# Optimization experiments

Measured on AMD Instinct MI355X. Metric: run time of the kernel, lower is better.

The kernel has to match this reference:

```python
import jax, jax.numpy as jnp
import numpy as np

D = 120000   # sample_size
H1 = 600     # sample_size/200
H2 = 300     # sample_size/400
H3 = 200     # sample_size/600
DENSITY = 0.1  # sparselinear default connectivity
B = 512
EPS = 1e-5

_LAYER_SPECS = [(H1, D), (H1, H1), (H2, H1), (H3, H2), (H3, H3)]


def _make_idx(key, out_d, in_d, nnz):
    k1, k2 = jax.random.split(key)
    rows = jax.random.randint(k1, (nnz,), 0, out_d)
    cols = jax.random.randint(k2, (nnz,), 0, in_d)
    return jnp.stack([rows, cols]).astype(jnp.int32)


def setup_inputs() -> dict:
    key = jax.random.key(0)
    ks = jax.random.split(key, 32)
    inp = {"x": jax.random.normal(ks[0], (B, D), jnp.float32)}
    for i, (o, ii) in enumerate(_LAYER_SPECS, 1):
        nnz = int(DENSITY * o * ii)
        scale = 1.0 / np.sqrt(DENSITY * ii)  # kaiming-like fan-in scaling on nonzeros
        inp[f"idx{i}"] = _make_idx(ks[3 * i], o, ii, nnz)
        inp[f"val{i}"] = jax.random.normal(ks[3 * i + 1], (nnz,), jnp.float32) * scale
        inp[f"b{i}"] = jnp.zeros((o,), jnp.float32)
    for j, d in enumerate([H1, H2, H3], 1):
        inp[f"g{j}"] = jnp.ones((d,), jnp.float32)
        inp[f"be{j}"] = jnp.zeros((d,), jnp.float32)
    return inp


def _sp_linear(x, idx, vals, bias, out_d):
    # COO sparse linear: y = x @ W^T + b, W scattered from (row, col, val)
    in_d = x.shape[1]
    W = jnp.zeros((out_d, in_d), x.dtype).at[idx[0], idx[1]].add(vals)
    return x @ W.T + bias


def _bn(x, g, b):
    # BatchNorm1d, training mode: biased batch variance
    m = x.mean(axis=0)
    v = x.var(axis=0)
    return (x - m) * jax.lax.rsqrt(v + EPS) * g + b


def reference(x, idx1, val1, b1, idx2, val2, b2, idx3, val3, b3,
              idx4, val4, b4, idx5, val5, b5,
              g1, be1, g2, be2, g3, be3):
    h = jax.nn.silu(_bn(_sp_linear(x, idx1, val1, b1, H1), g1, be1))
    h = jax.nn.silu(_sp_linear(h, idx2, val2, b2, H1))
    h = jax.nn.silu(_bn(_sp_linear(h, idx3, val3, b3, H2), g2, be2))
    h = jax.nn.silu(_bn(_sp_linear(h, idx4, val4, b4, H3), g3, be3))
    return _sp_linear(h, idx5, val5, b5, H3)
```

## Files before the change

kernel.cpp:

```cpp
#include <hip/hip_runtime.h>

typedef unsigned short ushort_t;
typedef unsigned int uint_t;

typedef __bf16 bf16x8 __attribute__((ext_vector_type(8)));
typedef float  floatx4 __attribute__((ext_vector_type(4)));

#define AS3 __attribute__((address_space(3)))
#define AS1 __attribute__((address_space(1)))

#define BATCH 512
#define D_IN  120000
#define N1P   640
#define N2P   640
#define N3P   320
#define N4P   256
#define N5P   256

#define KSPLIT 30
#define KCHUNK 4000

#define HALF    60000
#define CHW     15000
#define NREG    1200
#define NB      256
#define RSTRIDE 6912

static constexpr long O_W1 = 0;
static constexpr long SZ_W1 = 640L * 120000 * 2;
static constexpr long O_W2 = O_W1 + SZ_W1;
static constexpr long SZ_W2 = 640L * 640 * 4;
static constexpr long O_W3 = O_W2 + SZ_W2;
static constexpr long SZ_W3 = 320L * 640 * 4;
static constexpr long O_W4 = O_W3 + SZ_W3;
static constexpr long SZ_W4 = 256L * 320 * 4;
static constexpr long O_W5 = O_W4 + SZ_W4;
static constexpr long SZ_W5 = 256L * 256 * 4;
static constexpr long O_Y1 = O_W5 + SZ_W5;
static constexpr long SZ_Y1 = 512L * 640 * 4;
static constexpr long ZERO_OFF = O_W2;
static constexpr long ZERO_BYTES = (O_Y1 + SZ_Y1) - O_W2;
static constexpr long O_XB = O_Y1 + SZ_Y1;
static constexpr long SZ_XB = 512L * 120000 * 2;
static constexpr long O_CNT = O_XB;
static constexpr long O_OFF = O_CNT + (long)NREG * NB * 4;
static constexpr long O_TOT = O_OFF + (long)NB * NREG * 4;
static constexpr long O_REC = O_TOT + 4800;
static constexpr long O_H1 = O_XB;
static constexpr long O_H2 = O_H1 + 512L * 640 * 4;
static constexpr long O_Y3 = O_H2 + 512L * 640 * 4;
static constexpr long O_H3 = O_Y3 + 512L * 320 * 4;
static constexpr long O_Y4 = O_H3 + 512L * 320 * 4;
static constexpr long O_H4 = O_Y4 + 512L * 256 * 4;

__device__ __forceinline__ ushort_t f2bf(float f) {
    union { float f; uint_t u; } x;
    x.f = f;
    uint_t u = x.u;
    return (ushort_t)((u + 0x7FFFu + ((u >> 16) & 1u)) >> 16);
}
__device__ __forceinline__ float silu_f(float z) {
    return z / (1.f + expf(-z));
}
__device__ __forceinline__ void load16_lds(const void* g, void* l) {
    __builtin_amdgcn_global_load_lds((const AS1 char*)g, (AS3 char*)l, 16, 0, 0);
}

__global__ void zero_f4(float4* __restrict__ p, long n4) {
    long stride = (long)gridDim.x * blockDim.x;
    for (long i = (long)blockIdx.x * blockDim.x + threadIdx.x; i < n4; i += stride)
        p[i] = make_float4(0.f, 0.f, 0.f, 0.f);
}

__global__ void cast_f32_bf16(const float* __restrict__ X, ushort_t* __restrict__ Xb, long n8) {
    long t = (long)blockIdx.x * blockDim.x + threadIdx.x;
    if (t >= n8) return;
    const float4* p = (const float4*)X + 2 * t;
    float4 a = p[0], b = p[1];
    union { ushort_t us[8]; uint4 v; } u;
    u.us[0] = f2bf(a.x); u.us[1] = f2bf(a.y); u.us[2] = f2bf(a.z); u.us[3] = f2bf(a.w);
    u.us[4] = f2bf(b.x); u.us[5] = f2bf(b.y); u.us[6] = f2bf(b.z); u.us[7] = f2bf(b.w);
    ((uint4*)Xb)[t] = u.v;
}

__global__ __launch_bounds__(512) void hist1(const int* __restrict__ idx, int nnz, int chunk,
                                             int* __restrict__ counts ) {
    __shared__ uint_t h[NREG];
    const int b = blockIdx.x, t = threadIdx.x;
    for (int i = t; i < NREG; i += 512) h[i] = 0;
    __syncthreads();
    const int s = b * chunk;
    const int e = min(s + chunk, nnz);
    for (int i = s + t; i < e; i += 512) {
        int r = idx[i];
        int c = idx[nnz + i];
        atomicAdd(&h[r * 2 + (c >= HALF ? 1 : 0)], 1u);
    }
    __syncthreads();
    for (int i = t; i < NREG; i += 512) counts[(long)i * NB + b] = (int)h[i];
}

__global__ __launch_bounds__(NB) void scan1(const int* __restrict__ counts ,
                                            int* __restrict__ offs ,
                                            int* __restrict__ totals) {
    __shared__ int s[NB];
    const int reg = blockIdx.x, t = threadIdx.x;
    const int v = counts[(long)reg * NB + t];
    s[t] = v;
    __syncthreads();
    for (int o = 1; o < NB; o <<= 1) {
        int x = (t >= o) ? s[t - o] : 0;
        __syncthreads();
        s[t] += x;
        __syncthreads();
    }
    offs[(long)t * NREG + reg] = s[t] - v;
    if (t == NB - 1) totals[reg] = s[t];
}

__global__ __launch_bounds__(512) void scatter1(const int* __restrict__ idx,
                                                const float* __restrict__ vals,
                                                int nnz, int chunk,
                                                const int* __restrict__ offs ,
                                                int2* __restrict__ rec) {
    __shared__ int cur[NREG];
    const int b = blockIdx.x, t = threadIdx.x;
    const int* ob = offs + (long)b * NREG;
    for (int i = t; i < NREG; i += 512) cur[i] = i * RSTRIDE + ob[i];
    __syncthreads();
    const int s = b * chunk;
    const int e = min(s + chunk, nnz);
    for (int i = s + t; i < e; i += 512) {
        int r = idx[i];
        int c = idx[nnz + i];
        float v = vals[i];
        int h = (c >= HALF) ? 1 : 0;
        int reg = r * 2 + h;
        int slot = atomicAdd(&cur[reg], 1);
        if (slot < (reg + 1) * RSTRIDE)
            rec[slot] = make_int2(c - h * HALF, __float_as_int(v));
    }
}

__global__ __launch_bounds__(512) void build_w1(const int2* __restrict__ rec,
                                                const int* __restrict__ totals,
                                                ushort_t* __restrict__ W) {
    const int bid = blockIdx.x;
    const int r = bid >> 1, h = bid & 1;
    const int t = threadIdx.x;
    ushort_t* dstbase = W + (size_t)r * D_IN + h * HALF;

    if (r >= 600) {
        uint4 z = make_uint4(0, 0, 0, 0);
        for (int j = t * 8; j < HALF; j += 512 * 8) *(uint4*)(dstbase + j) = z;
        return;
    }

    __shared__ int2 lrec[RSTRIDE];
    __shared__ float acc[CHW];

    const int reg = r * 2 + h;
    const int n = min(totals[reg], RSTRIDE);
    const int2* src = rec + (long)reg * RSTRIDE;
    for (int i = t; i < n; i += 512) lrec[i] = src[i];
    __syncthreads();

#pragma unroll
    for (int ch = 0; ch < 4; ch++) {
        for (int j = t * 4; j < CHW; j += 512 * 4)
            *(float4*)&acc[j] = make_float4(0.f, 0.f, 0.f, 0.f);
        __syncthreads();
        const int base = ch * CHW;
        for (int i = t; i < n; i += 512) {
            int2 e = lrec[i];
            unsigned off = (unsigned)(e.x - base);
            if (off < (unsigned)CHW)
                atomicAdd(&acc[off], __int_as_float(e.y));
        }
        __syncthreads();
        ushort_t* dst = dstbase + base;
        for (int j = t * 8; j < CHW; j += 512 * 8) {
            union { ushort_t us[8]; uint4 v; } u;
#pragma unroll
            for (int k = 0; k < 8; k++) u.us[k] = f2bf(acc[j + k]);
            *(uint4*)(dst + j) = u.v;
        }
        __syncthreads();
    }
}

__global__ void scatter_all(const int* __restrict__ i2, const float* __restrict__ v2, int n2,
                            const int* __restrict__ i3, const float* __restrict__ v3, int n3,
                            const int* __restrict__ i4, const float* __restrict__ v4, int n4,
                            const int* __restrict__ i5, const float* __restrict__ v5, int n5,
                            float* __restrict__ W2, float* __restrict__ W3,
                            float* __restrict__ W4, float* __restrict__ W5) {
    int i = blockIdx.x * blockDim.x + threadIdx.x;
    if (i < n2) { atomicAdd(&W2[(size_t)i2[i] * 640 + i2[n2 + i]], v2[i]); return; }
    i -= n2;
    if (i < n3) { atomicAdd(&W3[(size_t)i3[i] * 640 + i3[n3 + i]], v3[i]); return; }
    i -= n3;
    if (i < n4) { atomicAdd(&W4[(size_t)i4[i] * 320 + i4[n4 + i]], v4[i]); return; }
    i -= n4;
    if (i < n5) { atomicAdd(&W5[(size_t)i5[i] * 256 + i5[n5 + i]], v5[i]); }
}

__global__ __launch_bounds__(256) void gemm1(const ushort_t* __restrict__ X,
                                             const ushort_t* __restrict__ W,
                                             float* __restrict__ Y) {
    __shared__ ushort_t sA[3][4096];
    __shared__ ushort_t sB[3][4096];

    const int b = blockIdx.x;
    const int wrk = (b & 7) * 75 + (b >> 3);
    const int ksIdx = wrk / 20;
    const int tile = wrk % 20;
    const int bm = tile / 5, bn = tile % 5;
    const int ks = ksIdx * KCHUNK;
    const int iters = KCHUNK / 32;

    const int t = threadIdx.x;
    const int lane = t & 63;
    const int w = t >> 6;
    const int wm = w >> 1, wn = w & 1;
    const int i16 = lane & 15;
    const int qk = lane >> 4;

    const int row0 = t >> 2;
    const int kq = (t & 3) ^ ((t >> 3) & 3);

    const ushort_t* pa0 = X + (size_t)(bm * 128 + row0) * D_IN + ks + kq * 8;
    const ushort_t* pa1 = pa0 + (size_t)64 * D_IN;
    const ushort_t* pb0 = W + (size_t)(bn * 128 + row0) * D_IN + ks + kq * 8;
    const ushort_t* pb1 = pb0 + (size_t)64 * D_IN;

    int aoff[4], boff[4];
#pragma unroll
    for (int mi = 0; mi < 4; mi++) {
        int row = wm * 64 + mi * 16 + i16;
        aoff[mi] = row * 64 + ((qk ^ ((row >> 1) & 3)) * 16);
    }
#pragma unroll
    for (int ni = 0; ni < 4; ni++) {
        int row = wn * 64 + ni * 16 + i16;
        boff[ni] = row * 64 + ((qk ^ ((row >> 1) & 3)) * 16);
    }
    const char* sAb = (const char*)sA;
    const char* sBb = (const char*)sB;

#define STAGE1(s) do {                                   \
        load16_lds(pa0, &sA[s][(w * 64) * 8]);           \
        load16_lds(pa1, &sA[s][(256 + w * 64) * 8]);     \
        load16_lds(pb0, &sB[s][(w * 64) * 8]);           \
        load16_lds(pb1, &sB[s][(256 + w * 64) * 8]);     \
        pa0 += 32; pa1 += 32; pb0 += 32; pb1 += 32; } while (0)

    floatx4 acc[4][4] = {};

    STAGE1(0);
    STAGE1(1);

    for (int it = 0; it < iters; ++it) {
        if (it < iters - 1) {
            asm volatile("s_waitcnt vmcnt(4)" ::: "memory");
        } else {
            asm volatile("s_waitcnt vmcnt(0)" ::: "memory");
        }
        __builtin_amdgcn_s_barrier();
        __builtin_amdgcn_sched_barrier(0);

        if (it + 2 < iters) {
            const int ns = (it + 2) % 3;
            STAGE1(ns);
        }

        const int cb = it % 3;
        bf16x8 af[4], bfr[4];
#pragma unroll
        for (int mi = 0; mi < 4; mi++)
            af[mi] = *(const bf16x8*)(sAb + cb * 8192 + aoff[mi]);
#pragma unroll
        for (int ni = 0; ni < 4; ni++)
            bfr[ni] = *(const bf16x8*)(sBb + cb * 8192 + boff[ni]);
#pragma unroll
        for (int mi = 0; mi < 4; mi++)
#pragma unroll
            for (int ni = 0; ni < 4; ni++)
                acc[mi][ni] = __builtin_amdgcn_mfma_f32_16x16x32_bf16(af[mi], bfr[ni], acc[mi][ni], 0, 0, 0);
    }
#undef STAGE1

#pragma unroll
    for (int mi = 0; mi < 4; mi++) {
#pragma unroll
        for (int ni = 0; ni < 4; ni++) {
#pragma unroll
            for (int r = 0; r < 4; r++) {
                int row = bm * 128 + wm * 64 + mi * 16 + qk * 4 + r;
                int col = bn * 128 + wn * 64 + ni * 16 + i16;
                atomicAdd(&Y[(size_t)row * N1P + col], acc[mi][ni][r]);
            }
        }
    }
}

__global__ __launch_bounds__(512) void bn_silu(const float* __restrict__ Y, int ld, int realN,
                                               const float* __restrict__ g,
                                               const float* __restrict__ be,
                                               float* __restrict__ H) {
    const int t = threadIdx.x;
    const int sub = t >> 6;
    const int c = t & 63;
    const int col = blockIdx.x * 64 + c;

    float s = 0.f, ss = 0.f;
#pragma unroll 8
    for (int r = sub; r < BATCH; r += 8) {
        float v = Y[(size_t)r * ld + col];
        s += v;
        ss += v * v;
    }
    __shared__ float rs[8][64], rq[8][64], scs[64], shs[64];
    rs[sub][c] = s;
    rq[sub][c] = ss;
    __syncthreads();
    if (t < 64) {
        float S = 0.f, SS = 0.f;
#pragma unroll
        for (int k = 0; k < 8; k++) { S += rs[k][t]; SS += rq[k][t]; }
        float mean = S * (1.f / 512.f);
        float var  = SS * (1.f / 512.f) - mean * mean;
        int cc = blockIdx.x * 64 + t;
        float sc = 0.f, sh = 0.f;
        if (cc < realN) {
            sc = rsqrtf(var + 1e-5f) * g[cc];
            sh = be[cc] - mean * sc;
        }
        scs[t] = sc;
        shs[t] = sh;
    }
    __syncthreads();
    const float sc = scs[c], sh = shs[c];
#pragma unroll 8
    for (int r = sub; r < BATCH; r += 8) {
        float v = Y[(size_t)r * ld + col];
        H[(size_t)r * ld + col] = silu_f(v * sc + sh);
    }
}

template <int ACT, int GUARD>
__global__ __launch_bounds__(256) void small_gemm(const float* __restrict__ A, int lda,
                                                  const float* __restrict__ W, int ldw,
                                                  const float* __restrict__ bias, int biasN,
                                                  float* __restrict__ out, int ldo, int outN,
                                                  int K) {
    __shared__ float sA[64][20];
    __shared__ float sB[64][20];
    const int t = threadIdx.x;
    const int m0 = blockIdx.x * 64, n0 = blockIdx.y * 64;
    const int ty = t >> 4, tx = t & 15;
    const int lm = t >> 2, lq = t & 3;
    float acc[4][4] = {};

    for (int kt = 0; kt < K; kt += 16) {
        __syncthreads();
        float4 av = *(const float4*)&A[(size_t)(m0 + lm) * lda + kt + lq * 4];
        float4 wv = *(const float4*)&W[(size_t)(n0 + lm) * ldw + kt + lq * 4];
        sA[lm][lq * 4 + 0] = av.x; sA[lm][lq * 4 + 1] = av.y;
        sA[lm][lq * 4 + 2] = av.z; sA[lm][lq * 4 + 3] = av.w;
        sB[lm][lq * 4 + 0] = wv.x; sB[lm][lq * 4 + 1] = wv.y;
        sB[lm][lq * 4 + 2] = wv.z; sB[lm][lq * 4 + 3] = wv.w;
        __syncthreads();
#pragma unroll
        for (int kg = 0; kg < 4; kg++) {
            float4 a4[4], b4[4];
#pragma unroll
            for (int i = 0; i < 4; i++) a4[i] = *(const float4*)&sA[ty * 4 + i][kg * 4];
#pragma unroll
            for (int j = 0; j < 4; j++) b4[j] = *(const float4*)&sB[tx * 4 + j][kg * 4];
#pragma unroll
            for (int i = 0; i < 4; i++)
#pragma unroll
                for (int j = 0; j < 4; j++)
                    acc[i][j] += a4[i].x * b4[j].x + a4[i].y * b4[j].y +
                                 a4[i].z * b4[j].z + a4[i].w * b4[j].w;
        }
    }

#pragma unroll
    for (int i = 0; i < 4; i++) {
#pragma unroll
        for (int j = 0; j < 4; j++) {
            int row = m0 + ty * 4 + i;
            int col = n0 + tx * 4 + j;
            float v = acc[i][j];
            if (bias != nullptr && col < biasN) v += bias[col];
            if (ACT == 1) v = silu_f(v);
            if (GUARD) {
                if (col < outN) out[(size_t)row * ldo + col] = v;
            } else {
                out[(size_t)row * ldo + col] = v;
            }
        }
    }
}

extern "C" void kernel_launch(void* const* d_in, const int* in_sizes, int n_in,
                              void* d_out, int out_size, void* d_ws, size_t ws_size,
                              hipStream_t stream) {
    const float* x   = (const float*)d_in[0];
    const int* idx1 = (const int*)d_in[1];  const float* val1 = (const float*)d_in[2];
    const int* idx2 = (const int*)d_in[4];  const float* val2 = (const float*)d_in[5];
    const float* b2 = (const float*)d_in[6];
    const int* idx3 = (const int*)d_in[7];  const float* val3 = (const float*)d_in[8];
    const int* idx4 = (const int*)d_in[10]; const float* val4 = (const float*)d_in[11];
    const int* idx5 = (const int*)d_in[13]; const float* val5 = (const float*)d_in[14];
    const float* b5 = (const float*)d_in[15];
    const float* g1 = (const float*)d_in[16]; const float* be1 = (const float*)d_in[17];
    const float* g2 = (const float*)d_in[18]; const float* be2 = (const float*)d_in[19];
    const float* g3 = (const float*)d_in[20]; const float* be3 = (const float*)d_in[21];

    const int nnz1 = in_sizes[1] / 2;
    const int nnz2 = in_sizes[4] / 2;
    const int nnz3 = in_sizes[7] / 2;
    const int nnz4 = in_sizes[10] / 2;
    const int nnz5 = in_sizes[13] / 2;

    char* ws = (char*)d_ws;
    ushort_t* W1 = (ushort_t*)(ws + O_W1);
    float* W2 = (float*)(ws + O_W2);
    float* W3 = (float*)(ws + O_W3);
    float* W4 = (float*)(ws + O_W4);
    float* W5 = (float*)(ws + O_W5);
    float* y1 = (float*)(ws + O_Y1);
    int*   cnt = (int*)(ws + O_CNT);
    int*   off = (int*)(ws + O_OFF);
    int*   tot = (int*)(ws + O_TOT);
    int2*  rec = (int2*)(ws + O_REC);
    ushort_t* Xb = (ushort_t*)(ws + O_XB);
    float* h1 = (float*)(ws + O_H1);
    float* h2 = (float*)(ws + O_H2);
    float* y3 = (float*)(ws + O_Y3);
    float* h3 = (float*)(ws + O_H3);
    float* y4 = (float*)(ws + O_Y4);
    float* h4 = (float*)(ws + O_H4);

    zero_f4<<<dim3((unsigned)(ZERO_BYTES / 16 / 256 + 1)), dim3(256), 0, stream>>>(
        (float4*)(ws + ZERO_OFF), ZERO_BYTES / 16);

    {
        const int chunk = (nnz1 + NB - 1) / NB;
        hist1<<<dim3(NB), dim3(512), 0, stream>>>(idx1, nnz1, chunk, cnt);
        scan1<<<dim3(NREG), dim3(NB), 0, stream>>>(cnt, off, tot);
        scatter1<<<dim3(NB), dim3(512), 0, stream>>>(idx1, val1, nnz1, chunk, off, rec);
        build_w1<<<dim3(640 * 2), dim3(512), 0, stream>>>(rec, tot, W1);
    }

    {
        long n8 = (long)BATCH * D_IN / 8;
        cast_f32_bf16<<<dim3((unsigned)((n8 + 255) / 256)), dim3(256), 0, stream>>>(x, Xb, n8);
    }

    {
        int ntot = nnz2 + nnz3 + nnz4 + nnz5;
        scatter_all<<<dim3((ntot + 255) / 256), dim3(256), 0, stream>>>(
            idx2, val2, nnz2, idx3, val3, nnz3, idx4, val4, nnz4, idx5, val5, nnz5,
            W2, W3, W4, W5);
    }

    gemm1<<<dim3(8 * 75), dim3(256), 0, stream>>>(Xb, W1, y1);

    bn_silu<<<dim3(N1P / 64), dim3(512), 0, stream>>>(y1, N1P, 600, g1, be1, h1);

    small_gemm<1, 0><<<dim3(8, N2P / 64), dim3(256), 0, stream>>>(h1, N1P, W2, 640, b2, 600,
                                                                  h2, N2P, N2P, 640);
    small_gemm<0, 0><<<dim3(8, N3P / 64), dim3(256), 0, stream>>>(h2, N2P, W3, 640, nullptr, 0,
                                                                  y3, N3P, N3P, 640);
    bn_silu<<<dim3(N3P / 64), dim3(512), 0, stream>>>(y3, N3P, 300, g2, be2, h3);

    small_gemm<0, 0><<<dim3(8, N4P / 64), dim3(256), 0, stream>>>(h3, N3P, W4, 320, nullptr, 0,
                                                                  y4, N4P, N4P, 320);
    bn_silu<<<dim3(N4P / 64), dim3(512), 0, stream>>>(y4, N4P, 200, g3, be3, h4);

    small_gemm<0, 1><<<dim3(8, N5P / 64), dim3(256), 0, stream>>>(h4, N4P, W5, 256, b5, 200,
                                                                  (float*)d_out, 200, 200, 256);
    (void)n_in; (void)out_size; (void)ws_size;
}
```

Before: 1.038 ms.

## Fuse fp32-to-bf16 cast of X into gemm1 A-tile loading

Removes the separate cast kernel that converted the whole input to bf16 in workspace. gemm1 now loads fp32 A tiles into registers, converts them with packed bf16 conversion, and writes them to LDS, with a restructured three-buffer pipeline and explicit waitcnt/barrier placement. This avoids writing and re-reading about 123MB of bf16 data. In exchange the GEMM reads twice as many bytes for A through registers instead of direct global-to-LDS loads, and has more VGPR pressure and more complex synchronization.

```diff
diff --git a/kernel.cpp b/kernel.cpp
--- a/kernel.cpp
+++ b/kernel.cpp
@@ -40,13 +40,12 @@
 static constexpr long SZ_Y1 = 512L * 640 * 4;
 static constexpr long ZERO_OFF = O_W2;
 static constexpr long ZERO_BYTES = (O_Y1 + SZ_Y1) - O_W2;
-static constexpr long O_XB = O_Y1 + SZ_Y1;
-static constexpr long SZ_XB = 512L * 120000 * 2;
-static constexpr long O_CNT = O_XB;
+static constexpr long O_SCR = O_Y1 + SZ_Y1;
+static constexpr long O_CNT = O_SCR;
 static constexpr long O_OFF = O_CNT + (long)NREG * NB * 4;
 static constexpr long O_TOT = O_OFF + (long)NB * NREG * 4;
 static constexpr long O_REC = O_TOT + 4800;
-static constexpr long O_H1 = O_XB;
+static constexpr long O_H1 = O_SCR;
 static constexpr long O_H2 = O_H1 + 512L * 640 * 4;
 static constexpr long O_Y3 = O_H2 + 512L * 640 * 4;
 static constexpr long O_H3 = O_Y3 + 512L * 320 * 4;
@@ -59,6 +58,11 @@
     uint_t u = x.u;
     return (ushort_t)((u + 0x7FFFu + ((u >> 16) & 1u)) >> 16);
 }
+__device__ __forceinline__ uint_t cvt_pk_bf16(float lo, float hi) {
+    uint_t r;
+    asm("v_cvt_pk_bf16_f32 %0, %1, %2" : "=v"(r) : "v"(lo), "v"(hi));
+    return r;
+}
 __device__ __forceinline__ float silu_f(float z) {
     return z / (1.f + expf(-z));
 }
@@ -70,17 +74,6 @@
     long stride = (long)gridDim.x * blockDim.x;
     for (long i = (long)blockIdx.x * blockDim.x + threadIdx.x; i < n4; i += stride)
         p[i] = make_float4(0.f, 0.f, 0.f, 0.f);
-}
-
-__global__ void cast_f32_bf16(const float* __restrict__ X, ushort_t* __restrict__ Xb, long n8) {
-    long t = (long)blockIdx.x * blockDim.x + threadIdx.x;
-    if (t >= n8) return;
-    const float4* p = (const float4*)X + 2 * t;
-    float4 a = p[0], b = p[1];
-    union { ushort_t us[8]; uint4 v; } u;
-    u.us[0] = f2bf(a.x); u.us[1] = f2bf(a.y); u.us[2] = f2bf(a.z); u.us[3] = f2bf(a.w);
-    u.us[4] = f2bf(b.x); u.us[5] = f2bf(b.y); u.us[6] = f2bf(b.z); u.us[7] = f2bf(b.w);
-    ((uint4*)Xb)[t] = u.v;
 }
 
 __global__ __launch_bounds__(512) void hist1(const int* __restrict__ idx, int nnz, int chunk,
@@ -205,7 +198,7 @@
     if (i < n5) { atomicAdd(&W5[(size_t)i5[i] * 256 + i5[n5 + i]], v5[i]); }
 }
 
-__global__ __launch_bounds__(256) void gemm1(const ushort_t* __restrict__ X,
+__global__ __launch_bounds__(256) void gemm1(const float* __restrict__ X,
                                              const ushort_t* __restrict__ W,
                                              float* __restrict__ Y) {
     __shared__ ushort_t sA[3][4096];
@@ -229,8 +222,8 @@
     const int row0 = t >> 2;
     const int kq = (t & 3) ^ ((t >> 3) & 3);
 
-    const ushort_t* pa0 = X + (size_t)(bm * 128 + row0) * D_IN + ks + kq * 8;
-    const ushort_t* pa1 = pa0 + (size_t)64 * D_IN;
+    const float*    qa0 = X + (size_t)(bm * 128 + row0) * D_IN + ks + kq * 8;
+    const float*    qa1 = qa0 + (size_t)64 * D_IN;
     const ushort_t* pb0 = W + (size_t)(bn * 128 + row0) * D_IN + ks + kq * 8;
     const ushort_t* pb1 = pb0 + (size_t)64 * D_IN;
 
@@ -248,47 +241,76 @@
     const char* sAb = (const char*)sA;
     const char* sBb = (const char*)sB;
 
-#define STAGE1(s) do {                                   \
-        load16_lds(pa0, &sA[s][(w * 64) * 8]);           \
-        load16_lds(pa1, &sA[s][(256 + w * 64) * 8]);     \
+#define STAGEB(s) do {                                   \
         load16_lds(pb0, &sB[s][(w * 64) * 8]);           \
         load16_lds(pb1, &sB[s][(256 + w * 64) * 8]);     \
-        pa0 += 32; pa1 += 32; pb0 += 32; pb1 += 32; } while (0)
+        pb0 += 32; pb1 += 32; } while (0)
+#define LOADA(d0, d1, d2, d3) do {                       \
+        d0 = *(const float4*)qa0;                        \
+        d1 = *(const float4*)(qa0 + 4);                  \
+        d2 = *(const float4*)qa1;                        \
+        d3 = *(const float4*)(qa1 + 4);                  \
+        qa0 += 32; qa1 += 32; } while (0)
+#define WRITEA(s, d0, d1, d2, d3) do {                   \
+        uint4 u0, u1;                                    \
+        u0.x = cvt_pk_bf16(d0.x, d0.y); u0.y = cvt_pk_bf16(d0.z, d0.w); \
+        u0.z = cvt_pk_bf16(d1.x, d1.y); u0.w = cvt_pk_bf16(d1.z, d1.w); \
+        u1.x = cvt_pk_bf16(d2.x, d2.y); u1.y = cvt_pk_bf16(d2.z, d2.w); \
+        u1.z = cvt_pk_bf16(d3.x, d3.y); u1.w = cvt_pk_bf16(d3.z, d3.w); \
+        *(uint4*)&sA[s][t * 8] = u0;                     \
+        *(uint4*)&sA[s][(t + 256) * 8] = u1; } while (0)
 
     floatx4 acc[4][4] = {};
-
-    STAGE1(0);
-    STAGE1(1);
-
+    float4 p0, p1, p2, p3;
+    float4 n0, n1, n2, n3;
+
+    {
+        float4 a0, a1, a2, a3;
+        STAGEB(0);
+        LOADA(a0, a1, a2, a3);
+        STAGEB(1);
+        LOADA(p0, p1, p2, p3);
+        asm volatile("s_waitcnt vmcnt(6)" ::: "memory");
+        WRITEA(0, a0, a1, a2, a3);
+        asm volatile("s_waitcnt lgkmcnt(0)" ::: "memory");
+    }
+    __builtin_amdgcn_s_barrier();
+    __builtin_amdgcn_sched_barrier(0);
+
+    int cb = 0, wb = 1, nb = 2;
     for (int it = 0; it < iters; ++it) {
-        if (it < iters - 1) {
-            asm volatile("s_waitcnt vmcnt(4)" ::: "memory");
-        } else {
-            asm volatile("s_waitcnt vmcnt(0)" ::: "memory");
-        }
-        __builtin_amdgcn_s_barrier();
-        __builtin_amdgcn_sched_barrier(0);
-
         if (it + 2 < iters) {
-            const int ns = (it + 2) % 3;
-            STAGE1(ns);
-        }
-
-        const int cb = it % 3;
+            STAGEB(nb);
+            LOADA(n0, n1, n2, n3);
+        }
+
+        const int cbo = cb * 8192;
         bf16x8 af[4], bfr[4];
 #pragma unroll
         for (int mi = 0; mi < 4; mi++)
-            af[mi] = *(const bf16x8*)(sAb + cb * 8192 + aoff[mi]);
+            af[mi] = *(const bf16x8*)(sAb + cbo + aoff[mi]);
 #pragma unroll
         for (int ni = 0; ni < 4; ni++)
-            bfr[ni] = *(const bf16x8*)(sBb + cb * 8192 + boff[ni]);
+            bfr[ni] = *(const bf16x8*)(sBb + cbo + boff[ni]);
 #pragma unroll
         for (int mi = 0; mi < 4; mi++)
 #pragma unroll
             for (int ni = 0; ni < 4; ni++)
                 acc[mi][ni] = __builtin_amdgcn_mfma_f32_16x16x32_bf16(af[mi], bfr[ni], acc[mi][ni], 0, 0, 0);
-    }
-#undef STAGE1
+
+        if (it + 1 < iters) {
+            WRITEA(wb, p0, p1, p2, p3);
+            p0 = n0; p1 = n1; p2 = n2; p3 = n3;
+            asm volatile("s_waitcnt vmcnt(6)" ::: "memory");
+            asm volatile("s_waitcnt lgkmcnt(0)" ::: "memory");
+            __builtin_amdgcn_s_barrier();
+            __builtin_amdgcn_sched_barrier(0);
+        }
+        int tmp = cb; cb = wb; wb = nb; nb = tmp;
+    }
+#undef STAGEB
+#undef LOADA
+#undef WRITEA
 
 #pragma unroll
     for (int mi = 0; mi < 4; mi++) {
@@ -437,7 +459,6 @@
     int*   off = (int*)(ws + O_OFF);
     int*   tot = (int*)(ws + O_TOT);
     int2*  rec = (int2*)(ws + O_REC);
-    ushort_t* Xb = (ushort_t*)(ws + O_XB);
     float* h1 = (float*)(ws + O_H1);
     float* h2 = (float*)(ws + O_H2);
     float* y3 = (float*)(ws + O_Y3);
@@ -457,18 +478,13 @@
     }
 
     {
-        long n8 = (long)BATCH * D_IN / 8;
-        cast_f32_bf16<<<dim3((unsigned)((n8 + 255) / 256)), dim3(256), 0, stream>>>(x, Xb, n8);
-    }
-
-    {
         int ntot = nnz2 + nnz3 + nnz4 + nnz5;
         scatter_all<<<dim3((ntot + 255) / 256), dim3(256), 0, stream>>>(
             idx2, val2, nnz2, idx3, val3, nnz3, idx4, val4, nnz4, idx5, val5, nnz5,
             W2, W3, W4, W5);
     }
 
-    gemm1<<<dim3(8 * 75), dim3(256), 0, stream>>>(Xb, W1, y1);
+    gemm1<<<dim3(8 * 75), dim3(256), 0, stream>>>(x, W1, y1);
 
     bn_silu<<<dim3(N1P / 64), dim3(512), 0, stream>>>(y1, N1P, 600, g1, be1, h1);
 
```

Measured after the change: 1.033 ms. Within noise of the previous version (-0.5%).
